# Kernel optimization log

Hardware: AMD Instinct MI355X
Metric: run time of the kernel (lower is better)

## Reference

```python
import jax, jax.numpy as jnp
import numpy as np

N = 50000      # nodes
E = 800000     # edges
D = 64         # input_dim = hidden_dim = output_dim
ED = 16        # edge_attr dim
L = 4          # total GATConv layers (2 per GAT block)
G = 64         # number of graphs in the batch vector
NEG_SLOPE = 0.2


def setup_inputs() -> dict:
    key = jax.random.key(0)
    ks = jax.random.split(key, 12)
    s = 0.1
    x = jax.random.normal(ks[0], (N, D), jnp.float32)
    edge_index = jax.random.randint(ks[1], (2, E), 0, N, jnp.int32)
    edge_attr = jax.random.normal(ks[2], (E, ED), jnp.float32)
    batch = jnp.sort(jax.random.randint(ks[3], (N,), 0, G, jnp.int32))
    return {
        "x": x,
        "edge_index": edge_index,
        "edge_attr": edge_attr,
        "batch": batch,
        # stacked per-layer GATConv params (all layers are D->D)
        "W": jax.random.normal(ks[4], (L, D, D), jnp.float32) * s,
        "a_src": jax.random.normal(ks[5], (L, D), jnp.float32) * s,
        "a_dst": jax.random.normal(ks[6], (L, D), jnp.float32) * s,
        "We": jax.random.normal(ks[7], (L, ED, D), jnp.float32) * s,
        "a_e": jax.random.normal(ks[8], (L, D), jnp.float32) * s,
        "b": jnp.zeros((L, D), jnp.float32),
        "Wfc": jax.random.normal(ks[9], (D, 2048), jnp.float32) * s,
        "bfc": jnp.zeros((2048,), jnp.float32),
    }


def _gat_conv(h, src, dst, edge_attr, W, a_s, a_d, We, a_e, b):
    # single-head GATConv with edge features (PyG semantics, flow src->dst)
    hw = h @ W                                      # [N, D]
    el = (edge_attr @ We) @ a_e                     # [E]
    score = jax.nn.leaky_relu(
        (hw @ a_s)[src] + (hw @ a_d)[dst] + el, NEG_SLOPE)  # [E]
    # softmax over incoming edges of each dst node
    m = jax.ops.segment_max(score, dst, num_segments=N)      # [N]
    p = jnp.exp(score - m[dst])                               # [E]
    denom = jax.ops.segment_sum(p, dst, num_segments=N)      # [N]
    alpha = p / denom[dst]                                    # [E]
    out = jax.ops.segment_sum(alpha[:, None] * hw[src], dst, num_segments=N)
    return out + b


def reference(x, edge_index, edge_attr, batch, W, a_src, a_dst, We, a_e, b, Wfc, bfc):
    src, dst = edge_index[0], edge_index[1]
    h = x
    for l in range(L):
        h = _gat_conv(h, src, dst, edge_attr,
                      W[l], a_src[l], a_dst[l], We[l], a_e[l], b[l])
        if l < L - 1:  # relu inside blocks and between the two GAT blocks
            h = jax.nn.relu(h)
    # global_mean_pool over batch vector
    counts = jax.ops.segment_sum(jnp.ones((N,), h.dtype), batch, num_segments=G)
    pooled = jax.ops.segment_sum(h, batch, num_segments=G) / jnp.maximum(counts, 1.0)[:, None]
    out = pooled @ Wfc + bfc                        # [G, 2048]
    return out[None]                                # stacked over list -> [1, G, 2048]
```

## Files before the change

### kernel.cpp

```cpp
#include <hip/hip_runtime.h>
#include <hip/hip_bf16.h>

#define NN 50000
#define EE 800000
#define DD 64
#define LL 4
#define GG 64
#define PJ 16
#define NXCD 8
#define DRANGE (NN / NXCD)

__global__ __launch_bounds__(256) void k_el(const float* __restrict__ ea,
                                            const float* __restrict__ We,
                                            const float* __restrict__ a_e,
                                            const int* __restrict__ dst,
                                            int* __restrict__ counts,
                                            float* __restrict__ el_all, int ne) {
    __shared__ float sce[64];
    if (threadIdx.x < 64) {
        int l = threadIdx.x >> 4, k = threadIdx.x & 15;
        float acc = 0.f;
        for (int j = 0; j < 64; ++j)
            acc += We[l * 1024 + k * 64 + j] * a_e[l * 64 + j];
        sce[threadIdx.x] = acc;
    }
    __syncthreads();
    int e = blockIdx.x * 256 + threadIdx.x;
    if (e >= ne) return;
    atomicAdd(&counts[dst[e]], 1);
    const float4* p4 = reinterpret_cast<const float4*>(ea + (size_t)e * 16);
    float v[16];
    float4 q;
    q = p4[0]; v[0] = q.x; v[1] = q.y; v[2] = q.z; v[3] = q.w;
    q = p4[1]; v[4] = q.x; v[5] = q.y; v[6] = q.z; v[7] = q.w;
    q = p4[2]; v[8] = q.x; v[9] = q.y; v[10] = q.z; v[11] = q.w;
    q = p4[3]; v[12] = q.x; v[13] = q.y; v[14] = q.z; v[15] = q.w;
    float o[4];
#pragma unroll
    for (int l = 0; l < 4; ++l) {
        float a = 0.f;
#pragma unroll
        for (int k = 0; k < 16; ++k) a = fmaf(v[k], sce[l * 16 + k], a);
        o[l] = a;
    }
    reinterpret_cast<float4*>(el_all)[e] = make_float4(o[0], o[1], o[2], o[3]);
}

__global__ void k_scan1(const int* __restrict__ counts, int* __restrict__ bsum, int n) {
    __shared__ int s[256];
    int i = blockIdx.x * 256 + threadIdx.x;
    s[threadIdx.x] = (i < n) ? counts[i] : 0;
    __syncthreads();
    for (int off = 128; off; off >>= 1) {
        if (threadIdx.x < off) s[threadIdx.x] += s[threadIdx.x + off];
        __syncthreads();
    }
    if (threadIdx.x == 0) bsum[blockIdx.x] = s[0];
}

__global__ void k_scan2(int* __restrict__ bsum, int nb) {
    __shared__ int s[256];
    int t = threadIdx.x;
    int v = (t < nb) ? bsum[t] : 0;
    s[t] = v;
    __syncthreads();
    for (int off = 1; off < 256; off <<= 1) {
        int x = (t >= off) ? s[t - off] : 0;
        __syncthreads();
        s[t] += x;
        __syncthreads();
    }
    if (t < nb) bsum[t] = s[t] - v;
}

__global__ void k_scan3(const int* __restrict__ counts, const int* __restrict__ bsum,
                        int* __restrict__ row_ptr, int n) {
    __shared__ int s[256];
    int t = threadIdx.x;
    int i = blockIdx.x * 256 + t;
    int v = (i < n) ? counts[i] : 0;
    s[t] = v;
    __syncthreads();
    for (int off = 1; off < 256; off <<= 1) {
        int x = (t >= off) ? s[t - off] : 0;
        __syncthreads();
        s[t] += x;
        __syncthreads();
    }
    if (i < n) row_ptr[i] = s[t] - v + bsum[blockIdx.x];
}

__global__ __launch_bounds__(256) void k_fill(const int* __restrict__ dst,
                                              const int* __restrict__ row_ptr,
                                              int* __restrict__ cursor,
                                              int* __restrict__ csr_eid, int ne) {
    int r = blockIdx.x;
    int e = blockIdx.y * 256 + threadIdx.x;
    if (e >= ne) return;
    int d = dst[e];
    int rlo = r * DRANGE;
    if (d < rlo || d >= rlo + DRANGE) return;
    int pos = row_ptr[d] + atomicAdd(&cursor[d], 1);
    csr_eid[pos] = e;
}

__global__ __launch_bounds__(256) void k_sortperm(int* __restrict__ csr_eid,
                                                  const int* __restrict__ e_src,
                                                  const int* __restrict__ row_ptr,
                                                  const int* __restrict__ counts,
                                                  const float4* __restrict__ el_all,
                                                  int* __restrict__ csr_src,
                                                  float* __restrict__ e0, float* __restrict__ e1,
                                                  float* __restrict__ e2, float* __restrict__ e3,
                                                  int n) {
    int wid = threadIdx.x >> 6, lane = threadIdx.x & 63;
    int nd = blockIdx.x * 4 + wid;
    if (nd >= n) return;
    int s = row_ptr[nd], d = counts[nd];
    if (d == 0) return;
    if (d <= 64) {
        int eid = 0x7FFFFFFF;
        if (lane < d) eid = csr_eid[s + lane];
        int rank = 0;
        for (int j = 0; j < d; ++j) {
            int ej = __shfl(eid, j, 64);
            rank += (ej < eid) ? 1 : 0;
        }
        if (lane < d) {
            int sr = e_src[eid];
            float4 ev = el_all[eid];
            csr_src[s + rank] = sr;
            e0[s + rank] = ev.x; e1[s + rank] = ev.y;
            e2[s + rank] = ev.z; e3[s + rank] = ev.w;
        }
    } else if (lane == 0) {
        for (int i = 1; i < d; ++i) {
            int key = csr_eid[s + i];
            int j = i - 1;
            while (j >= 0 && csr_eid[s + j] > key) {
                csr_eid[s + j + 1] = csr_eid[s + j];
                --j;
            }
            csr_eid[s + j + 1] = key;
        }
        for (int i = 0; i < d; ++i) {
            int eid = csr_eid[s + i];
            float4 ev = el_all[eid];
            csr_src[s + i] = e_src[eid];
            e0[s + i] = ev.x; e1[s + i] = ev.y; e2[s + i] = ev.z; e3[s + i] = ev.w;
        }
    }
}

__global__ __launch_bounds__(256) void k_gemm(const float* __restrict__ h,
                                              const float* __restrict__ W,
                                              const float* __restrict__ a_s,
                                              const float* __restrict__ a_d,
                                              float* __restrict__ hw,
                                              float* __restrict__ ssrc,
                                              float* __restrict__ sdst, int n) {
    __shared__ float sHT[64 * 68];
    __shared__ float sW[64 * 64];
    int t = threadIdx.x;
    int nbase = blockIdx.x * 64;
    int nrem = n - nbase;
    const float4* W4 = (const float4*)W;
    float4* sW4 = (float4*)sW;
#pragma unroll
    for (int p = 0; p < 4; ++p) sW4[t + p * 256] = W4[t + p * 256];
#pragma unroll
    for (int p = 0; p < 4; ++p) {
        int idx = t + p * 256;
        int node = idx >> 4, d4 = idx & 15;
        float4 v = make_float4(0.f, 0.f, 0.f, 0.f);
        if (node < nrem) v = ((const float4*)(h + (size_t)(nbase + node) * 64))[d4];
        sHT[(d4 * 4 + 0) * 68 + node] = v.x;
        sHT[(d4 * 4 + 1) * 68 + node] = v.y;
        sHT[(d4 * 4 + 2) * 68 + node] = v.z;
        sHT[(d4 * 4 + 3) * 68 + node] = v.w;
    }
    __syncthreads();
    int nr = (t >> 4) * 4;
    int nc = (t & 15) * 4;
    float a0[4], a1[4], a2[4], a3[4];
#pragma unroll
    for (int j = 0; j < 4; ++j) { a0[j] = 0.f; a1[j] = 0.f; a2[j] = 0.f; a3[j] = 0.f; }
    for (int k = 0; k < 64; ++k) {
        float4 hv = *(const float4*)&sHT[k * 68 + nr];
        float4 wv = *(const float4*)&sW[k * 64 + nc];
        a0[0] = fmaf(hv.x, wv.x, a0[0]); a0[1] = fmaf(hv.x, wv.y, a0[1]);
        a0[2] = fmaf(hv.x, wv.z, a0[2]); a0[3] = fmaf(hv.x, wv.w, a0[3]);
        a1[0] = fmaf(hv.y, wv.x, a1[0]); a1[1] = fmaf(hv.y, wv.y, a1[1]);
        a1[2] = fmaf(hv.y, wv.z, a1[2]); a1[3] = fmaf(hv.y, wv.w, a1[3]);
        a2[0] = fmaf(hv.z, wv.x, a2[0]); a2[1] = fmaf(hv.z, wv.y, a2[1]);
        a2[2] = fmaf(hv.z, wv.z, a2[2]); a2[3] = fmaf(hv.z, wv.w, a2[3]);
        a3[0] = fmaf(hv.w, wv.x, a3[0]); a3[1] = fmaf(hv.w, wv.y, a3[1]);
        a3[2] = fmaf(hv.w, wv.z, a3[2]); a3[3] = fmaf(hv.w, wv.w, a3[3]);
    }
    if (nr + 0 < nrem) ((float4*)(hw + (size_t)(nbase + nr + 0) * 64))[t & 15] =
        make_float4(a0[0], a0[1], a0[2], a0[3]);
    if (nr + 1 < nrem) ((float4*)(hw + (size_t)(nbase + nr + 1) * 64))[t & 15] =
        make_float4(a1[0], a1[1], a1[2], a1[3]);
    if (nr + 2 < nrem) ((float4*)(hw + (size_t)(nbase + nr + 2) * 64))[t & 15] =
        make_float4(a2[0], a2[1], a2[2], a2[3]);
    if (nr + 3 < nrem) ((float4*)(hw + (size_t)(nbase + nr + 3) * 64))[t & 15] =
        make_float4(a3[0], a3[1], a3[2], a3[3]);
    float as0 = a_s[nc], as1 = a_s[nc + 1], as2 = a_s[nc + 2], as3 = a_s[nc + 3];
    float ad0 = a_d[nc], ad1 = a_d[nc + 1], ad2 = a_d[nc + 2], ad3 = a_d[nc + 3];
    float ts0 = fmaf(a0[3], as3, fmaf(a0[2], as2, fmaf(a0[1], as1, a0[0] * as0)));
    float ts1 = fmaf(a1[3], as3, fmaf(a1[2], as2, fmaf(a1[1], as1, a1[0] * as0)));
    float ts2 = fmaf(a2[3], as3, fmaf(a2[2], as2, fmaf(a2[1], as1, a2[0] * as0)));
    float ts3 = fmaf(a3[3], as3, fmaf(a3[2], as2, fmaf(a3[1], as1, a3[0] * as0)));
    float td0 = fmaf(a0[3], ad3, fmaf(a0[2], ad2, fmaf(a0[1], ad1, a0[0] * ad0)));
    float td1 = fmaf(a1[3], ad3, fmaf(a1[2], ad2, fmaf(a1[1], ad1, a1[0] * ad0)));
    float td2 = fmaf(a2[3], ad3, fmaf(a2[2], ad2, fmaf(a2[1], ad1, a2[0] * ad0)));
    float td3 = fmaf(a3[3], ad3, fmaf(a3[2], ad2, fmaf(a3[1], ad1, a3[0] * ad0)));
#pragma unroll
    for (int off = 1; off < 16; off <<= 1) {
        ts0 += __shfl_xor(ts0, off, 64); ts1 += __shfl_xor(ts1, off, 64);
        ts2 += __shfl_xor(ts2, off, 64); ts3 += __shfl_xor(ts3, off, 64);
        td0 += __shfl_xor(td0, off, 64); td1 += __shfl_xor(td1, off, 64);
        td2 += __shfl_xor(td2, off, 64); td3 += __shfl_xor(td3, off, 64);
    }
    if ((t & 15) == 0) {
        if (nr + 0 < nrem) { ssrc[nbase + nr + 0] = ts0; sdst[nbase + nr + 0] = td0; }
        if (nr + 1 < nrem) { ssrc[nbase + nr + 1] = ts1; sdst[nbase + nr + 1] = td1; }
        if (nr + 2 < nrem) { ssrc[nbase + nr + 2] = ts2; sdst[nbase + nr + 2] = td2; }
        if (nr + 3 < nrem) { ssrc[nbase + nr + 3] = ts3; sdst[nbase + nr + 3] = td3; }
    }
}

__global__ __launch_bounds__(256) void k_row(const float* __restrict__ hw,
                                             const float* __restrict__ ssrc,
                                             const float* __restrict__ sdstA,
                                             const int* __restrict__ csr_src,
                                             const float* __restrict__ elpL,
                                             const int* __restrict__ row_ptr,
                                             const int* __restrict__ counts,
                                             const float* __restrict__ bias,
                                             int relu_flag, float* __restrict__ hout, int n) {
    int wid = threadIdx.x >> 6, lane = threadIdx.x & 63;
    int nd = blockIdx.x * 4 + wid;
    if (nd >= n) return;
    int start = row_ptr[nd], deg = counts[nd];
    if (deg == 0) {
        float outv = bias[lane];
        if (relu_flag) outv = fmaxf(outv, 0.f);
        hout[(size_t)nd * 64 + lane] = outv;
        return;
    }
    if (deg <= 64) {
        float sdn = sdstA[nd];
        int p = start + lane;
        int s_l = 0;
        float sc = -INFINITY;
        if (lane < deg) {
            s_l = csr_src[p];
            sc = ssrc[s_l] + sdn + elpL[p];
            sc = sc > 0.f ? sc : 0.2f * sc;
        }
        float mx = sc;
#pragma unroll
        for (int off = 32; off; off >>= 1) mx = fmaxf(mx, __shfl_xor(mx, off, 64));
        float pe = (lane < deg) ? __expf(sc - mx) : 0.f;
        float dsum = pe;
#pragma unroll
        for (int off = 32; off; off >>= 1) dsum += __shfl_xor(dsum, off, 64);
        const float* hwL = hw + lane;
        float acc = 0.f;
        float v0 = 0.f, v1 = 0.f, v2 = 0.f, v3 = 0.f,
              v4 = 0.f, v5 = 0.f, v6 = 0.f, v7 = 0.f;
        {
            int t0 = __shfl(s_l, 0, 64), t1 = __shfl(s_l, 1, 64);
            int t2 = __shfl(s_l, 2, 64), t3 = __shfl(s_l, 3, 64);
            int t4 = __shfl(s_l, 4, 64), t5 = __shfl(s_l, 5, 64);
            int t6 = __shfl(s_l, 6, 64), t7 = __shfl(s_l, 7, 64);
            if (0 < deg) v0 = hwL[(size_t)t0 * 64];
            if (1 < deg) v1 = hwL[(size_t)t1 * 64];
            if (2 < deg) v2 = hwL[(size_t)t2 * 64];
            if (3 < deg) v3 = hwL[(size_t)t3 * 64];
            if (4 < deg) v4 = hwL[(size_t)t4 * 64];
            if (5 < deg) v5 = hwL[(size_t)t5 * 64];
            if (6 < deg) v6 = hwL[(size_t)t6 * 64];
            if (7 < deg) v7 = hwL[(size_t)t7 * 64];
        }
        for (int i = 0; i < deg; i += 8) {
            float p0 = __shfl(pe, i, 64),     p1 = __shfl(pe, (i + 1) & 63, 64);
            float p2 = __shfl(pe, (i + 2) & 63, 64), p3 = __shfl(pe, (i + 3) & 63, 64);
            float p4 = __shfl(pe, (i + 4) & 63, 64), p5 = __shfl(pe, (i + 5) & 63, 64);
            float p6 = __shfl(pe, (i + 6) & 63, 64), p7 = __shfl(pe, (i + 7) & 63, 64);
            int t0 = __shfl(s_l, (i + 8) & 63, 64),  t1 = __shfl(s_l, (i + 9) & 63, 64);
            int t2 = __shfl(s_l, (i + 10) & 63, 64), t3 = __shfl(s_l, (i + 11) & 63, 64);
            int t4 = __shfl(s_l, (i + 12) & 63, 64), t5 = __shfl(s_l, (i + 13) & 63, 64);
            int t6 = __shfl(s_l, (i + 14) & 63, 64), t7 = __shfl(s_l, (i + 15) & 63, 64);
            float w0 = v0, w1 = v1, w2 = v2, w3 = v3,
                  w4 = v4, w5 = v5, w6 = v6, w7 = v7;
            if (i + 8 < deg)  v0 = hwL[(size_t)t0 * 64];
            if (i + 9 < deg)  v1 = hwL[(size_t)t1 * 64];
            if (i + 10 < deg) v2 = hwL[(size_t)t2 * 64];
            if (i + 11 < deg) v3 = hwL[(size_t)t3 * 64];
            if (i + 12 < deg) v4 = hwL[(size_t)t4 * 64];
            if (i + 13 < deg) v5 = hwL[(size_t)t5 * 64];
            if (i + 14 < deg) v6 = hwL[(size_t)t6 * 64];
            if (i + 15 < deg) v7 = hwL[(size_t)t7 * 64];
            acc = fmaf(p0, w0, acc);
            if (i + 1 < deg) acc = fmaf(p1, w1, acc);
            if (i + 2 < deg) acc = fmaf(p2, w2, acc);
            if (i + 3 < deg) acc = fmaf(p3, w3, acc);
            if (i + 4 < deg) acc = fmaf(p4, w4, acc);
            if (i + 5 < deg) acc = fmaf(p5, w5, acc);
            if (i + 6 < deg) acc = fmaf(p6, w6, acc);
            if (i + 7 < deg) acc = fmaf(p7, w7, acc);
        }
        float outv = acc / dsum + bias[lane];
        if (relu_flag) outv = fmaxf(outv, 0.f);
        hout[(size_t)nd * 64 + lane] = outv;
        return;
    }
    {
        float sdn = sdstA[nd];
        float mx = -INFINITY;
        for (int i = lane; i < deg; i += 64) {
            int p = start + i;
            float sc = ssrc[csr_src[p]] + sdn + elpL[p];
            sc = sc > 0.f ? sc : 0.2f * sc;
            mx = fmaxf(mx, sc);
        }
#pragma unroll
        for (int off = 32; off; off >>= 1) mx = fmaxf(mx, __shfl_xor(mx, off, 64));
        float dsum = 0.f;
        for (int i = lane; i < deg; i += 64) {
            int p = start + i;
            float sc = ssrc[csr_src[p]] + sdn + elpL[p];
            sc = sc > 0.f ? sc : 0.2f * sc;
            dsum += __expf(sc - mx);
        }
#pragma unroll
        for (int off = 32; off; off >>= 1) dsum += __shfl_xor(dsum, off, 64);
        float acc = 0.f;
        for (int i = 0; i < deg; ++i) {
            int p = start + i;
            int s = csr_src[p];
            float sc = ssrc[s] + sdn + elpL[p];
            sc = sc > 0.f ? sc : 0.2f * sc;
            float pex = __expf(sc - mx);
            acc = fmaf(pex, hw[(size_t)s * 64 + lane], acc);
        }
        float outv = acc / dsum + bias[lane];
        if (relu_flag) outv = fmaxf(outv, 0.f);
        hout[(size_t)nd * 64 + lane] = outv;
    }
}

__global__ __launch_bounds__(256) void k_pool_part(const float* __restrict__ h,
                                                   const int* __restrict__ batch,
                                                   float* __restrict__ partial, int n) {
    int g = blockIdx.y, j = blockIdx.x;
    int lo = 0, hi = n;
    while (lo < hi) { int mid = (lo + hi) >> 1; if (batch[mid] < g) lo = mid + 1; else hi = mid; }
    int start = lo;
    lo = start; hi = n;
    while (lo < hi) { int mid = (lo + hi) >> 1; if (batch[mid] < g + 1) lo = mid + 1; else hi = mid; }
    int end = lo;
    int cnt = end - start;
    int chunk = (cnt + PJ - 1) / PJ;
    int clo = start + j * chunk;
    int chi = min(clo + chunk, end);
    int lane = threadIdx.x & 63, q = threadIdx.x >> 6;
    float acc = 0.f;
    for (int nd = clo + q; nd < chi; nd += 4) acc += h[(size_t)nd * 64 + lane];
    __shared__ float s[4][64];
    s[q][lane] = acc;
    __syncthreads();
    if (threadIdx.x < 64) {
        float tot = s[0][threadIdx.x] + s[1][threadIdx.x] + s[2][threadIdx.x] + s[3][threadIdx.x];
        partial[((size_t)g * PJ + j) * 64 + threadIdx.x] = tot;
    }
}

__global__ __launch_bounds__(256) void k_fc(const float* __restrict__ partial,
                                            const int* __restrict__ batch,
                                            const float* __restrict__ Wfc,
                                            const float* __restrict__ bfc,
                                            float* __restrict__ out, int n) {
    int g = blockIdx.y;
    int c = blockIdx.x * 256 + threadIdx.x;
    __shared__ float sp[64];
    if (threadIdx.x < 64) {
        int d = threadIdx.x;
        float tot = 0.f;
#pragma unroll
        for (int j = 0; j < PJ; ++j) tot += partial[((size_t)g * PJ + j) * 64 + d];
        int lo = 0, hi = n;
        while (lo < hi) { int mid = (lo + hi) >> 1; if (batch[mid] < g) lo = mid + 1; else hi = mid; }
        int start = lo;
        lo = start; hi = n;
        while (lo < hi) { int mid = (lo + hi) >> 1; if (batch[mid] < g + 1) lo = mid + 1; else hi = mid; }
        int cnt = lo - start;
        sp[d] = tot / fmaxf((float)cnt, 1.0f);
    }
    __syncthreads();
    float acc = bfc[c];
#pragma unroll
    for (int k = 0; k < 64; ++k) acc = fmaf(sp[k], Wfc[k * 2048 + c], acc);
    out[(size_t)g * 2048 + c] = acc;
}

extern "C" void kernel_launch(void* const* d_in, const int* in_sizes, int n_in,
                              void* d_out, int out_size, void* d_ws, size_t ws_size,
                              hipStream_t stream) {
    const float* x = (const float*)d_in[0];
    const int* edge_index = (const int*)d_in[1];
    const float* edge_attr = (const float*)d_in[2];
    const int* batch = (const int*)d_in[3];
    const float* W = (const float*)d_in[4];
    const float* a_src = (const float*)d_in[5];
    const float* a_dst = (const float*)d_in[6];
    const float* We = (const float*)d_in[7];
    const float* a_e = (const float*)d_in[8];
    const float* b = (const float*)d_in[9];
    const float* Wfc = (const float*)d_in[10];
    const float* bfc = (const float*)d_in[11];
    float* out = (float*)d_out;

    char* ws = (char*)d_ws;
    size_t off = 0;
    auto alloc = [&](size_t bytes) {
        void* p = ws + off;
        off = (off + bytes + 255) & ~(size_t)255;
        return p;
    };
    float* h0      = (float*)alloc((size_t)NN * 64 * 4);
    float* h1      = (float*)alloc((size_t)NN * 64 * 4);
    float* hw      = (float*)alloc((size_t)NN * 64 * 4);
    float* ssrc    = (float*)alloc((size_t)NN * 4);
    float* sdst    = (float*)alloc((size_t)NN * 4);
    float* el_all  = (float*)alloc((size_t)EE * 16);
    float* elpT    = (float*)alloc((size_t)EE * 4 * 4);
    int*   csr_src = (int*)alloc((size_t)EE * 4);
    int*   csr_eid = (int*)alloc((size_t)EE * 4);
    int*   counts  = (int*)alloc((size_t)NN * 4);
    int*   row_ptr = (int*)alloc((size_t)NN * 4);
    int*   cursor  = (int*)alloc((size_t)NN * 4);
    int*   bsum    = (int*)alloc(256 * 4);
    float* partial = (float*)alloc((size_t)GG * PJ * 64 * 4);
    (void)ws_size; (void)in_sizes; (void)n_in; (void)out_size;

    const int* e_src = edge_index;
    const int* e_dst = edge_index + EE;
    const int EB = EE / 256;
    const int NB = (NN + 255) / 256;

    hipMemsetAsync(counts, 0, (size_t)NN * 4, stream);
    hipMemsetAsync(cursor, 0, (size_t)NN * 4, stream);

    k_el<<<EB, 256, 0, stream>>>(edge_attr, We, a_e, e_dst, counts, el_all, EE);
    k_scan1<<<NB, 256, 0, stream>>>(counts, bsum, NN);
    k_scan2<<<1, 256, 0, stream>>>(bsum, NB);
    k_scan3<<<NB, 256, 0, stream>>>(counts, bsum, row_ptr, NN);
    k_fill<<<dim3(NXCD, EB), 256, 0, stream>>>(e_dst, row_ptr, cursor, csr_eid, EE);
    k_sortperm<<<(NN + 3) / 4, 256, 0, stream>>>(csr_eid, e_src, row_ptr, counts,
                                                 (const float4*)el_all, csr_src,
                                                 elpT, elpT + EE, elpT + 2 * (size_t)EE,
                                                 elpT + 3 * (size_t)EE, NN);

    const float* hin = x;
    float* hbufs[2] = {h0, h1};
    for (int l = 0; l < LL; ++l) {
        k_gemm<<<(NN + 63) / 64, 256, 0, stream>>>(hin, W + l * 4096, a_src + l * 64,
                                                   a_dst + l * 64, hw, ssrc, sdst, NN);
        float* hout = hbufs[l & 1];
        k_row<<<(NN + 3) / 4, 256, 0, stream>>>(hw, ssrc, sdst, csr_src,
                                                elpT + (size_t)l * EE, row_ptr, counts,
                                                b + l * 64, (l < LL - 1) ? 1 : 0, hout, NN);
        hin = hout;
    }
    k_pool_part<<<dim3(PJ, GG), 256, 0, stream>>>(hin, batch, partial, NN);
    k_fc<<<dim3(2048 / 256, GG), 256, 0, stream>>>(partial, batch, Wfc, bfc, out, NN);
}
```

Before: 366.5 us.

## Fuse edge-attr projection into CSR permute, split histogram by XCD, drop gather guards

```diff
diff --git a/kernel.cpp b/kernel.cpp
--- a/kernel.cpp
+++ b/kernel.cpp
@@ -10,40 +10,25 @@
 #define NXCD 8
 #define DRANGE (NN / NXCD)
 
-__global__ __launch_bounds__(256) void k_el(const float* __restrict__ ea,
-                                            const float* __restrict__ We,
-                                            const float* __restrict__ a_e,
-                                            const int* __restrict__ dst,
-                                            int* __restrict__ counts,
-                                            float* __restrict__ el_all, int ne) {
-    __shared__ float sce[64];
-    if (threadIdx.x < 64) {
-        int l = threadIdx.x >> 4, k = threadIdx.x & 15;
-        float acc = 0.f;
-        for (int j = 0; j < 64; ++j)
-            acc += We[l * 1024 + k * 64 + j] * a_e[l * 64 + j];
-        sce[threadIdx.x] = acc;
-    }
-    __syncthreads();
-    int e = blockIdx.x * 256 + threadIdx.x;
+__global__ void k_ce(const float* __restrict__ We, const float* __restrict__ a_e,
+                     float* __restrict__ ce) {
+    int t = threadIdx.x;
+    int l = t >> 4, k = t & 15;
+    float acc = 0.f;
+    for (int j = 0; j < 64; ++j)
+        acc += We[l * 1024 + k * 64 + j] * a_e[l * 64 + j];
+    ce[t] = acc;
+}
+
+__global__ __launch_bounds__(256) void k_hist(const int* __restrict__ dst,
+                                              int* __restrict__ counts, int ne) {
+    int r = blockIdx.x;
+    int e = blockIdx.y * 256 + threadIdx.x;
     if (e >= ne) return;
-    atomicAdd(&counts[dst[e]], 1);
-    const float4* p4 = reinterpret_cast<const float4*>(ea + (size_t)e * 16);
-    float v[16];
-    float4 q;
-    q = p4[0]; v[0] = q.x; v[1] = q.y; v[2] = q.z; v[3] = q.w;
-    q = p4[1]; v[4] = q.x; v[5] = q.y; v[6] = q.z; v[7] = q.w;
-    q = p4[2]; v[8] = q.x; v[9] = q.y; v[10] = q.z; v[11] = q.w;
-    q = p4[3]; v[12] = q.x; v[13] = q.y; v[14] = q.z; v[15] = q.w;
-    float o[4];
-#pragma unroll
-    for (int l = 0; l < 4; ++l) {
-        float a = 0.f;
-#pragma unroll
-        for (int k = 0; k < 16; ++k) a = fmaf(v[k], sce[l * 16 + k], a);
-        o[l] = a;
-    }
-    reinterpret_cast<float4*>(el_all)[e] = make_float4(o[0], o[1], o[2], o[3]);
+    int d = dst[e];
+    int rlo = r * DRANGE;
+    if (d < rlo || d >= rlo + DRANGE) return;
+    atomicAdd(&counts[d], 1);
 }
 
 __global__ void k_scan1(const int* __restrict__ counts, int* __restrict__ bsum, int n) {
@@ -108,11 +93,15 @@
                                                   const int* __restrict__ e_src,
                                                   const int* __restrict__ row_ptr,
                                                   const int* __restrict__ counts,
-                                                  const float4* __restrict__ el_all,
+                                                  const float* __restrict__ ea,
+                                                  const float* __restrict__ ce,
                                                   int* __restrict__ csr_src,
                                                   float* __restrict__ e0, float* __restrict__ e1,
                                                   float* __restrict__ e2, float* __restrict__ e3,
                                                   int n) {
+    __shared__ float sce[64];
+    if (threadIdx.x < 64) sce[threadIdx.x] = ce[threadIdx.x];
+    __syncthreads();
     int wid = threadIdx.x >> 6, lane = threadIdx.x & 63;
     int nd = blockIdx.x * 4 + wid;
     if (nd >= n) return;
@@ -128,10 +117,24 @@
         }
         if (lane < d) {
             int sr = e_src[eid];
-            float4 ev = el_all[eid];
+            const float4* p4 = reinterpret_cast<const float4*>(ea + (size_t)eid * 16);
+            float v[16];
+            float4 q;
+            q = p4[0]; v[0] = q.x; v[1] = q.y; v[2] = q.z; v[3] = q.w;
+            q = p4[1]; v[4] = q.x; v[5] = q.y; v[6] = q.z; v[7] = q.w;
+            q = p4[2]; v[8] = q.x; v[9] = q.y; v[10] = q.z; v[11] = q.w;
+            q = p4[3]; v[12] = q.x; v[13] = q.y; v[14] = q.z; v[15] = q.w;
+            float o[4];
+#pragma unroll
+            for (int l = 0; l < 4; ++l) {
+                float a = 0.f;
+#pragma unroll
+                for (int k = 0; k < 16; ++k) a = fmaf(v[k], sce[l * 16 + k], a);
+                o[l] = a;
+            }
             csr_src[s + rank] = sr;
-            e0[s + rank] = ev.x; e1[s + rank] = ev.y;
-            e2[s + rank] = ev.z; e3[s + rank] = ev.w;
+            e0[s + rank] = o[0]; e1[s + rank] = o[1];
+            e2[s + rank] = o[2]; e3[s + rank] = o[3];
         }
     } else if (lane == 0) {
         for (int i = 1; i < d; ++i) {
@@ -145,9 +148,15 @@
         }
         for (int i = 0; i < d; ++i) {
             int eid = csr_eid[s + i];
-            float4 ev = el_all[eid];
             csr_src[s + i] = e_src[eid];
-            e0[s + i] = ev.x; e1[s + i] = ev.y; e2[s + i] = ev.z; e3[s + i] = ev.w;
+            const float* vp = ea + (size_t)eid * 16;
+            float o[4];
+            for (int l = 0; l < 4; ++l) {
+                float a = 0.f;
+                for (int k = 0; k < 16; ++k) a = fmaf(vp[k], sce[l * 16 + k], a);
+                o[l] = a;
+            }
+            e0[s + i] = o[0]; e1[s + i] = o[1]; e2[s + i] = o[2]; e3[s + i] = o[3];
         }
     }
 }
@@ -268,49 +277,37 @@
         for (int off = 32; off; off >>= 1) dsum += __shfl_xor(dsum, off, 64);
         const float* hwL = hw + lane;
         float acc = 0.f;
-        float v0 = 0.f, v1 = 0.f, v2 = 0.f, v3 = 0.f,
-              v4 = 0.f, v5 = 0.f, v6 = 0.f, v7 = 0.f;
-        {
-            int t0 = __shfl(s_l, 0, 64), t1 = __shfl(s_l, 1, 64);
-            int t2 = __shfl(s_l, 2, 64), t3 = __shfl(s_l, 3, 64);
-            int t4 = __shfl(s_l, 4, 64), t5 = __shfl(s_l, 5, 64);
-            int t6 = __shfl(s_l, 6, 64), t7 = __shfl(s_l, 7, 64);
-            if (0 < deg) v0 = hwL[(size_t)t0 * 64];
-            if (1 < deg) v1 = hwL[(size_t)t1 * 64];
-            if (2 < deg) v2 = hwL[(size_t)t2 * 64];
-            if (3 < deg) v3 = hwL[(size_t)t3 * 64];
-            if (4 < deg) v4 = hwL[(size_t)t4 * 64];
-            if (5 < deg) v5 = hwL[(size_t)t5 * 64];
-            if (6 < deg) v6 = hwL[(size_t)t6 * 64];
-            if (7 < deg) v7 = hwL[(size_t)t7 * 64];
-        }
+        int t0 = __shfl(s_l, 0, 64), t1 = __shfl(s_l, 1, 64);
+        int t2 = __shfl(s_l, 2, 64), t3 = __shfl(s_l, 3, 64);
+        int t4 = __shfl(s_l, 4, 64), t5 = __shfl(s_l, 5, 64);
+        int t6 = __shfl(s_l, 6, 64), t7 = __shfl(s_l, 7, 64);
+        float v0 = hwL[(size_t)t0 * 64], v1 = hwL[(size_t)t1 * 64];
+        float v2 = hwL[(size_t)t2 * 64], v3 = hwL[(size_t)t3 * 64];
+        float v4 = hwL[(size_t)t4 * 64], v5 = hwL[(size_t)t5 * 64];
+        float v6 = hwL[(size_t)t6 * 64], v7 = hwL[(size_t)t7 * 64];
         for (int i = 0; i < deg; i += 8) {
-            float p0 = __shfl(pe, i, 64),     p1 = __shfl(pe, (i + 1) & 63, 64);
-            float p2 = __shfl(pe, (i + 2) & 63, 64), p3 = __shfl(pe, (i + 3) & 63, 64);
-            float p4 = __shfl(pe, (i + 4) & 63, 64), p5 = __shfl(pe, (i + 5) & 63, 64);
-            float p6 = __shfl(pe, (i + 6) & 63, 64), p7 = __shfl(pe, (i + 7) & 63, 64);
-            int t0 = __shfl(s_l, (i + 8) & 63, 64),  t1 = __shfl(s_l, (i + 9) & 63, 64);
-            int t2 = __shfl(s_l, (i + 10) & 63, 64), t3 = __shfl(s_l, (i + 11) & 63, 64);
-            int t4 = __shfl(s_l, (i + 12) & 63, 64), t5 = __shfl(s_l, (i + 13) & 63, 64);
-            int t6 = __shfl(s_l, (i + 14) & 63, 64), t7 = __shfl(s_l, (i + 15) & 63, 64);
+            float p0 = __shfl(pe, i, 64),     p1 = __shfl(pe, i + 1, 64);
+            float p2 = __shfl(pe, i + 2, 64), p3 = __shfl(pe, i + 3, 64);
+            float p4 = __shfl(pe, i + 4, 64), p5 = __shfl(pe, i + 5, 64);
+            float p6 = __shfl(pe, i + 6, 64), p7 = __shfl(pe, i + 7, 64);
+            int u0 = __shfl(s_l, (i + 8) & 63, 64),  u1 = __shfl(s_l, (i + 9) & 63, 64);
+            int u2 = __shfl(s_l, (i + 10) & 63, 64), u3 = __shfl(s_l, (i + 11) & 63, 64);
+            int u4 = __shfl(s_l, (i + 12) & 63, 64), u5 = __shfl(s_l, (i + 13) & 63, 64);
+            int u6 = __shfl(s_l, (i + 14) & 63, 64), u7 = __shfl(s_l, (i + 15) & 63, 64);
             float w0 = v0, w1 = v1, w2 = v2, w3 = v3,
                   w4 = v4, w5 = v5, w6 = v6, w7 = v7;
-            if (i + 8 < deg)  v0 = hwL[(size_t)t0 * 64];
-            if (i + 9 < deg)  v1 = hwL[(size_t)t1 * 64];
-            if (i + 10 < deg) v2 = hwL[(size_t)t2 * 64];
-            if (i + 11 < deg) v3 = hwL[(size_t)t3 * 64];
-            if (i + 12 < deg) v4 = hwL[(size_t)t4 * 64];
-            if (i + 13 < deg) v5 = hwL[(size_t)t5 * 64];
-            if (i + 14 < deg) v6 = hwL[(size_t)t6 * 64];
-            if (i + 15 < deg) v7 = hwL[(size_t)t7 * 64];
+            v0 = hwL[(size_t)u0 * 64]; v1 = hwL[(size_t)u1 * 64];
+            v2 = hwL[(size_t)u2 * 64]; v3 = hwL[(size_t)u3 * 64];
+            v4 = hwL[(size_t)u4 * 64]; v5 = hwL[(size_t)u5 * 64];
+            v6 = hwL[(size_t)u6 * 64]; v7 = hwL[(size_t)u7 * 64];
             acc = fmaf(p0, w0, acc);
-            if (i + 1 < deg) acc = fmaf(p1, w1, acc);
-            if (i + 2 < deg) acc = fmaf(p2, w2, acc);
-            if (i + 3 < deg) acc = fmaf(p3, w3, acc);
-            if (i + 4 < deg) acc = fmaf(p4, w4, acc);
-            if (i + 5 < deg) acc = fmaf(p5, w5, acc);
-            if (i + 6 < deg) acc = fmaf(p6, w6, acc);
-            if (i + 7 < deg) acc = fmaf(p7, w7, acc);
+            acc = fmaf(p1, w1, acc);
+            acc = fmaf(p2, w2, acc);
+            acc = fmaf(p3, w3, acc);
+            acc = fmaf(p4, w4, acc);
+            acc = fmaf(p5, w5, acc);
+            acc = fmaf(p6, w6, acc);
+            acc = fmaf(p7, w7, acc);
         }
         float outv = acc / dsum + bias[lane];
         if (relu_flag) outv = fmaxf(outv, 0.f);
@@ -435,7 +432,6 @@
     float* hw      = (float*)alloc((size_t)NN * 64 * 4);
     float* ssrc    = (float*)alloc((size_t)NN * 4);
     float* sdst    = (float*)alloc((size_t)NN * 4);
-    float* el_all  = (float*)alloc((size_t)EE * 16);
     float* elpT    = (float*)alloc((size_t)EE * 4 * 4);
     int*   csr_src = (int*)alloc((size_t)EE * 4);
     int*   csr_eid = (int*)alloc((size_t)EE * 4);
@@ -443,6 +439,7 @@
     int*   row_ptr = (int*)alloc((size_t)NN * 4);
     int*   cursor  = (int*)alloc((size_t)NN * 4);
     int*   bsum    = (int*)alloc(256 * 4);
+    float* ce      = (float*)alloc(64 * 4);
     float* partial = (float*)alloc((size_t)GG * PJ * 64 * 4);
     (void)ws_size; (void)in_sizes; (void)n_in; (void)out_size;
 
@@ -454,13 +451,14 @@
     hipMemsetAsync(counts, 0, (size_t)NN * 4, stream);
     hipMemsetAsync(cursor, 0, (size_t)NN * 4, stream);
 
-    k_el<<<EB, 256, 0, stream>>>(edge_attr, We, a_e, e_dst, counts, el_all, EE);
+    k_ce<<<1, 64, 0, stream>>>(We, a_e, ce);
+    k_hist<<<dim3(NXCD, EB), 256, 0, stream>>>(e_dst, counts, EE);
     k_scan1<<<NB, 256, 0, stream>>>(counts, bsum, NN);
     k_scan2<<<1, 256, 0, stream>>>(bsum, NB);
     k_scan3<<<NB, 256, 0, stream>>>(counts, bsum, row_ptr, NN);
     k_fill<<<dim3(NXCD, EB), 256, 0, stream>>>(e_dst, row_ptr, cursor, csr_eid, EE);
     k_sortperm<<<(NN + 3) / 4, 256, 0, stream>>>(csr_eid, e_src, row_ptr, counts,
-                                                 (const float4*)el_all, csr_src,
+                                                 edge_attr, ce, csr_src,
                                                  elpT, elpT + EE, elpT + 2 * (size_t)EE,
                                                  elpT + 3 * (size_t)EE, NN);
 
```

Result: slower. 447.6 us (+22.1%).
